# Kernel optimization log

Measured on AMD Instinct MI355X. Metric: run time of the kernel, lower is better.

## Reference

```python
import jax, jax.numpy as jnp
import numpy as np

NX = NY = NZ = 256   # linear_freqs
D1 = D2 = D3 = 8     # reduced_freqs
DF = 16              # feature_dim
NPTS = 131072


def softplus_b10(x):
    # torch F.softplus(x, beta=10, threshold=1)
    bx = 10.0 * x
    return jnp.where(bx > 1.0, x, 0.1 * jnp.log1p(jnp.exp(jnp.minimum(bx, 30.0))))


def grid_sample2d(vol, gx, gy):
    """Bilinear grid_sample, align_corners=True. vol:[C,H,W] (complex ok),
    gx,gy:[N] in [-1,1] (gx indexes W, gy indexes H). Returns [C,N]."""
    C, H, W = vol.shape
    ix = (gx + 1.0) * 0.5 * (W - 1)
    iy = (gy + 1.0) * 0.5 * (H - 1)
    x0f = jnp.floor(ix)
    y0f = jnp.floor(iy)
    wx = ix - x0f
    wy = iy - y0f
    x0 = jnp.clip(x0f.astype(jnp.int32), 0, W - 1)
    x1 = jnp.clip(x0 + 1, 0, W - 1)
    y0 = jnp.clip(y0f.astype(jnp.int32), 0, H - 1)
    y1 = jnp.clip(y0 + 1, 0, H - 1)
    v00 = vol[:, y0, x0]
    v01 = vol[:, y0, x1]
    v10 = vol[:, y1, x0]
    v11 = vol[:, y1, x1]
    return (v00 * (1 - wy) * (1 - wx) + v01 * (1 - wy) * wx
            + v10 * wy * (1 - wx) + v11 * wy * wx)


def batch_irfft(ph, x, ff, T):
    """ph:[D,d,N] complex, x:[N] in [-1,1], ff:[d] freqs. Returns [D,N]."""
    xx = (x + 1.0) * 0.5 * (T - 1) / T                    # [N]
    ang = 2.0 * np.pi * xx[:, None] * ff[None, :]         # [N,d]
    scale = jnp.where(ff > 0, 2.0, 1.0)
    tw_re = jnp.cos(ang) * scale
    tw_im = jnp.sin(ang) * scale
    return (jnp.einsum('dfn,nf->dn', ph.real, tw_re)
            - jnp.einsum('dfn,nf->dn', ph.imag, tw_im))


def setup_inputs() -> dict:
    key = jax.random.key(0)
    ks = jax.random.split(key, 8)
    inputs = jax.random.uniform(ks[0], (NPTS, 3), jnp.float32, minval=-1.0, maxval=1.0)
    s = 0.01
    Fx_re = jax.random.normal(ks[1], (1, DF, D1, NY, NZ), jnp.float32) * s
    Fx_im = jax.random.normal(ks[2], (1, DF, D1, NY, NZ), jnp.float32) * s
    Fy_re = jax.random.normal(ks[3], (1, DF, NX, D2, NZ), jnp.float32) * s
    Fy_im = jax.random.normal(ks[4], (1, DF, NX, D2, NZ), jnp.float32) * s
    Fz_re = jax.random.normal(ks[5], (1, DF, NX, NY, D3), jnp.float32) * s
    Fz_im = jax.random.normal(ks[6], (1, DF, NX, NY, D3), jnp.float32) * s
    alpha_params = jnp.array([0.001], jnp.float32)
    return {"inputs": inputs, "Fx_re": Fx_re, "Fx_im": Fx_im,
            "Fy_re": Fy_re, "Fy_im": Fy_im, "Fz_re": Fz_re, "Fz_im": Fz_im,
            "alpha_params": alpha_params}


def reference(inputs, Fx_re, Fx_im, Fy_re, Fy_im, Fz_re, Fz_im, alpha_params):
    alpha = softplus_b10(alpha_params)[0]
    Fx = (Fx_re + 1j * Fx_im) * alpha        # [1,D,d1,Ny,Nz]
    Fy = (Fy_re + 1j * Fy_im) * alpha        # [1,D,Nx,d2,Nz]
    Fz = (Fz_re + 1j * Fz_im) * alpha        # [1,D,Nx,Ny,d3]
    # inverse FFT over the two full (linear) spectral axes
    Fx = jnp.fft.ifftn(Fx, axes=(3, 4), norm='forward')
    Fy = jnp.fft.ifftn(Fy, axes=(2, 4), norm='forward')
    Fz = jnp.fft.ifftn(Fz, axes=(2, 3), norm='forward')
    xs, ys, zs = inputs[:, 0], inputs[:, 1], inputs[:, 2]
    N = inputs.shape[0]
    kx = jnp.arange(D1, dtype=jnp.float32)   # linear sampling axis [0,1,...]
    ky = jnp.arange(D2, dtype=jnp.float32)
    kz = jnp.arange(D3, dtype=jnp.float32)
    # complex bilinear gathers (H,W) = (Ny,Nz) / (Nx,Nz) / (Ny,Nx)
    fx = grid_sample2d(Fx.reshape(DF * D1, NY, NZ), zs, ys).reshape(DF, D1, N)
    fy = grid_sample2d(jnp.transpose(Fy, (0, 1, 3, 2, 4)).reshape(DF * D2, NX, NZ),
                       zs, xs).reshape(DF, D2, N)
    fz = grid_sample2d(jnp.transpose(Fz, (0, 1, 4, 3, 2)).reshape(DF * D3, NY, NX),
                       xs, ys).reshape(DF, D3, N)
    fxx = batch_irfft(fx, xs, kx, NX)
    fyy = batch_irfft(fy, ys, ky, NY)
    fzz = batch_irfft(fz, zs, kz, NZ)
    return (fxx + fyy + fzz).T               # [N, DF]
```

## Files before the change

kernel.cpp:

```cpp
#include <hip/hip_runtime.h>
#include <hip/hip_fp16.h>
#include <math.h>

#define NPTS 131072
#define RS 265
#define NBIN 65536

__device__ __forceinline__ float dev_alpha(const float* __restrict__ ap) {
    float x = ap[0];
    float bx = 10.0f * x;
    if (bx > 1.0f) return x;
    float e = expf(fminf(bx, 30.0f));
    return 0.1f * log1pf(e);
}

__device__ __forceinline__ void fft16_reg(float* re, float* im) {
    #define SW(a,b) { float t=re[a]; re[a]=re[b]; re[b]=t; t=im[a]; im[a]=im[b]; im[b]=t; }
    SW(1,8) SW(2,4) SW(3,12) SW(5,10) SW(7,14) SW(11,13)
    #undef SW
    const float C[8] = {1.f, 0.9238795325112867f, 0.7071067811865476f, 0.3826834323650898f,
                        0.f, -0.3826834323650898f, -0.7071067811865476f, -0.9238795325112867f};
    const float S[8] = {0.f, 0.3826834323650898f, 0.7071067811865476f, 0.9238795325112867f,
                        1.f, 0.9238795325112867f, 0.7071067811865476f, 0.3826834323650898f};
    #pragma unroll
    for (int m = 1; m < 16; m <<= 1) {
        #pragma unroll
        for (int k = 0; k < 16; k += 2 * m) {
            #pragma unroll
            for (int j = 0; j < m; ++j) {
                float wc = C[j * (8 / m)], ws = S[j * (8 / m)];
                int i0 = k + j, i1 = i0 + m;
                float tr = re[i1] * wc - im[i1] * ws;
                float ti = re[i1] * ws + im[i1] * wc;
                re[i1] = re[i0] - tr; im[i1] = im[i0] - ti;
                re[i0] += tr;         im[i0] += ti;
            }
        }
    }
}

__device__ __forceinline__ void fft256_block(float* lre, float* lim, int tid) {
    const int r = tid >> 4, s = tid & 15;
    float xr[16], xi[16];
    #pragma unroll
    for (int a = 0; a < 16; ++a) {
        xr[a] = lre[r * RS + 16 * a + s];
        xi[a] = lim[r * RS + 16 * a + s];
    }
    __syncthreads();
    fft16_reg(xr, xi);
    #pragma unroll
    for (int c = 0; c < 16; ++c) {
        float sn, cs;
        __sincosf(0.0245436926061703f * (float)(s * c), &sn, &cs);
        float tr = xr[c] * cs - xi[c] * sn;
        float ti = xr[c] * sn + xi[c] * cs;
        int idx = r * RS + 16 * c + (s ^ c);
        lre[idx] = tr; lim[idx] = ti;
    }
    __syncthreads();
    #pragma unroll
    for (int b = 0; b < 16; ++b) {
        int idx = r * RS + 16 * s + (b ^ s);
        xr[b] = lre[idx]; xi[b] = lim[idx];
    }
    __syncthreads();
    fft16_reg(xr, xi);
    #pragma unroll
    for (int d = 0; d < 16; ++d) {
        int idx = r * RS + 16 * d + s;
        lre[idx] = xr[d]; lim[idx] = xi[d];
    }
    __syncthreads();
}

__global__ __launch_bounds__(256) void fft_pass1_xy(
    const float* __restrict__ Fre, const float* __restrict__ Fim,
    const float* __restrict__ alpha_p, __half2* __restrict__ GT,
    int Sd, int Sa)
{
    __shared__ float lre[16 * RS], lim[16 * RS];
    const int tid = threadIdx.x, bg = blockIdx.x;
    const int d = bg & 7, ag = (bg >> 3) & 15, f = bg >> 7;
    const int a0 = ag * 16, c = f * 8 + d;
    const int base = f * 524288 + d * Sd + a0 * Sa;
    const float alpha = dev_alpha(alpha_p);
    for (int i = tid; i < 4096; i += 256) {
        int ar = i >> 8, b = i & 255;
        int addr = base + ar * Sa + b;
        lre[ar * RS + b] = Fre[addr] * alpha;
        lim[ar * RS + b] = Fim[addr] * alpha;
    }
    __syncthreads();
    fft256_block(lre, lim, tid);
    for (int i = tid; i < 4096; i += 256) {
        int k = i >> 4, rr = i & 15;
        GT[(c * 256 + k) * 256 + a0 + rr] = __floats2half2_rn(lre[rr * RS + k], lim[rr * RS + k]);
    }
}

__global__ __launch_bounds__(256) void fft_pass2_xy(
    const __half2* __restrict__ GT, __half2* __restrict__ V)
{
    __shared__ float lre[16 * RS], lim[16 * RS];
    const int tid = threadIdx.x, bg = blockIdx.x;
    const int cg = bg & 7, b = bg >> 3, c0 = cg * 16;
    for (int i = tid; i < 4096; i += 256) {
        int cr = i >> 8, a = i & 255;
        float2 v = __half22float2(GT[((c0 + cr) * 256 + b) * 256 + a]);
        lre[cr * RS + a] = v.x;
        lim[cr * RS + a] = v.y;
    }
    __syncthreads();
    fft256_block(lre, lim, tid);
    for (int i = tid; i < 4096; i += 256) {
        int k = i >> 4, cr = i & 15;
        V[(b * 256 + k) * 128 + c0 + cr] = __floats2half2_rn(lre[cr * RS + k], lim[cr * RS + k]);
    }
}

__global__ __launch_bounds__(256) void fft_pass1_z(
    const float* __restrict__ Fre, const float* __restrict__ Fim,
    const float* __restrict__ alpha_p, __half2* __restrict__ GTz)
{
    __shared__ float lre[16 * RS], lim[16 * RS];
    const int tid = threadIdx.x, bg = blockIdx.x;
    const int f = bg >> 7, kxp = bg & 127;
    const int base = f * 524288 + kxp * 4096;
    const float alpha = dev_alpha(alpha_p);
    for (int i = tid; i < 4096; i += 256) {
        int kxo = i >> 11, rem = i & 2047;
        int ky = rem >> 3, d = rem & 7;
        int row = kxo * 8 + d;
        lre[row * RS + ky] = Fre[base + i] * alpha;
        lim[row * RS + ky] = Fim[base + i] * alpha;
    }
    __syncthreads();
    fft256_block(lre, lim, tid);
    for (int i = tid; i < 4096; i += 256) {
        int k = i >> 4, rr = i & 15;
        GTz[k * 32768 + f * 2048 + kxp * 16 + rr] = __floats2half2_rn(lre[rr * RS + k], lim[rr * RS + k]);
    }
}

__global__ __launch_bounds__(256) void fft_pass2_z(
    const __half2* __restrict__ GTz, __half2* __restrict__ Vz)
{
    __shared__ float lre[16 * RS], lim[16 * RS];
    const int tid = threadIdx.x, bg = blockIdx.x;
    const int fp = bg & 7, b = bg >> 3;
    const int base = b * 32768 + fp * 4096;
    for (int i = tid; i < 4096; i += 256) {
        int fo = i >> 11, rem = i & 2047;
        int kx = rem >> 3, d = rem & 7;
        int row = fo * 8 + d;
        float2 v = __half22float2(GTz[base + i]);
        lre[row * RS + kx] = v.x;
        lim[row * RS + kx] = v.y;
    }
    __syncthreads();
    fft256_block(lre, lim, tid);
    for (int i = tid; i < 4096; i += 256) {
        int k = i >> 4, rr = i & 15;
        Vz[(b * 256 + k) * 128 + fp * 16 + rr] = __floats2half2_rn(lre[rr * RS + k], lim[rr * RS + k]);
    }
}

__device__ __forceinline__ int bin8(float v) {
    return min(max((int)((v + 1.0f) * 127.5f), 0), 255);
}
__device__ __forceinline__ int pt_key(const float* pts, int pid) {
    float y = pts[pid * 3 + 1], z = pts[pid * 3 + 2];
    return bin8(z) * 256 + bin8(y);
}

__global__ __launch_bounds__(256) void zero_hist(unsigned* __restrict__ h) {
    h[blockIdx.x * 256 + threadIdx.x] = 0;
}
__global__ __launch_bounds__(256) void hist_k(const float* __restrict__ pts, unsigned* __restrict__ h) {
    int pid = blockIdx.x * 256 + threadIdx.x;
    atomicAdd(&h[pt_key(pts, pid)], 1u);
}
__global__ __launch_bounds__(256) void scan_k(const unsigned* __restrict__ h, unsigned* __restrict__ cur) {
    __shared__ unsigned part[256];
    const int t = threadIdx.x;
    unsigned sum = 0;
    for (int i = 0; i < 256; ++i) sum += h[t * 256 + i];
    part[t] = sum;
    __syncthreads();
    for (int o = 1; o < 256; o <<= 1) {
        unsigned v = part[t];
        unsigned add = (t >= o) ? part[t - o] : 0u;
        __syncthreads();
        part[t] = v + add;
        __syncthreads();
    }
    unsigned run = (t > 0) ? part[t - 1] : 0u;
    for (int i = 0; i < 256; ++i) {
        cur[t * 256 + i] = run;
        run += h[t * 256 + i];
    }
}
__global__ __launch_bounds__(256) void scatter_k(const float* __restrict__ pts,
                                                 unsigned* __restrict__ cur,
                                                 unsigned* __restrict__ perm) {
    int pid = blockIdx.x * 256 + threadIdx.x;
    unsigned pos = atomicAdd(&cur[pt_key(pts, pid)], 1u);
    perm[pos] = (unsigned)pid;
}

__device__ __forceinline__ float4 bsample(const uint2* __restrict__ V,
                                          float gx, float gy, bool swap, int lane) {
    float ix = (gx + 1.0f) * 127.5f;
    float iy = (gy + 1.0f) * 127.5f;
    float x0f = floorf(ix), y0f = floorf(iy);
    float wx = ix - x0f, wy = iy - y0f;
    int x0 = min(max((int)x0f, 0), 255);
    int x1 = min(x0 + 1, 255);
    int y0 = min(max((int)y0f, 0), 255);
    int y1 = min(y0 + 1, 255);
    int rA, rB, rC, rD;
    if (swap) { rA = y0 * 256 + x0; rB = y0 * 256 + x1; rC = y1 * 256 + x0; rD = y1 * 256 + x1; }
    else      { rA = x0 * 256 + y0; rB = x1 * 256 + y0; rC = x0 * 256 + y1; rD = x1 * 256 + y1; }
    float w00 = (1.0f - wy) * (1.0f - wx);
    float w01 = (1.0f - wy) * wx;
    float w10 = wy * (1.0f - wx);
    float w11 = wy * wx;
    uint2 a = V[rA * 64 + lane];
    uint2 b = V[rB * 64 + lane];
    uint2 cc = V[rC * 64 + lane];
    uint2 dd = V[rD * 64 + lane];
    float4 s = make_float4(0.f, 0.f, 0.f, 0.f);
    float2 f0, f1;
    f0 = __half22float2(__builtin_bit_cast(__half2, a.x));  f1 = __half22float2(__builtin_bit_cast(__half2, a.y));
    s.x += w00 * f0.x; s.y += w00 * f0.y; s.z += w00 * f1.x; s.w += w00 * f1.y;
    f0 = __half22float2(__builtin_bit_cast(__half2, b.x));  f1 = __half22float2(__builtin_bit_cast(__half2, b.y));
    s.x += w01 * f0.x; s.y += w01 * f0.y; s.z += w01 * f1.x; s.w += w01 * f1.y;
    f0 = __half22float2(__builtin_bit_cast(__half2, cc.x)); f1 = __half22float2(__builtin_bit_cast(__half2, cc.y));
    s.x += w10 * f0.x; s.y += w10 * f0.y; s.z += w10 * f1.x; s.w += w10 * f1.y;
    f0 = __half22float2(__builtin_bit_cast(__half2, dd.x)); f1 = __half22float2(__builtin_bit_cast(__half2, dd.y));
    s.x += w11 * f0.x; s.y += w11 * f0.y; s.z += w11 * f1.x; s.w += w11 * f1.y;
    return s;
}

__device__ __forceinline__ float irdft(float4 s, float tw, int lane) {
    const float TWO_PI = 6.28318530717958647692f;
    float xx = (tw + 1.0f) * 0.5f * (255.0f / 256.0f);
    int k0 = (lane & 3) * 2;
    float sa, ca, sb, cb;
    __sincosf(TWO_PI * xx * (float)k0,       &sa, &ca);
    __sincosf(TWO_PI * xx * (float)(k0 + 1), &sb, &cb);
    float sc0 = (k0 > 0) ? 2.0f : 1.0f;
    return sc0 * (s.x * ca - s.y * sa) + 2.0f * (s.z * cb - s.w * sb);
}

__global__ __launch_bounds__(256) void sample_all(
    const uint2* __restrict__ Vx, const uint2* __restrict__ Vy, const uint2* __restrict__ Vz,
    const float* __restrict__ pts, const unsigned* __restrict__ perm,
    float* __restrict__ out)
{
    const int wid  = (int)((blockIdx.x * blockDim.x + threadIdx.x) >> 6);
    const int lane = threadIdx.x & 63;
    if (wid >= NPTS) return;
    const int pid = perm ? (int)perm[wid] : wid;
    const float xs = pts[pid * 3 + 0];
    const float ys = pts[pid * 3 + 1];
    const float zs = pts[pid * 3 + 2];

    float4 sx = bsample(Vx, zs, ys, false, lane);
    float4 sy = bsample(Vy, zs, xs, false, lane);
    float4 sz = bsample(Vz, xs, ys, true, lane);

    float p = irdft(sx, xs, lane) + irdft(sy, ys, lane) + irdft(sz, zs, lane);
    p += __shfl_xor(p, 1, 64);
    p += __shfl_xor(p, 2, 64);
    if ((lane & 3) == 0) out[pid * 16 + (lane >> 2)] = p;
}

extern "C" void kernel_launch(void* const* d_in, const int* in_sizes, int n_in,
                              void* d_out, int out_size, void* d_ws, size_t ws_size,
                              hipStream_t stream) {
    const float* pts     = (const float*)d_in[0];
    const float* Fx_re   = (const float*)d_in[1];
    const float* Fx_im   = (const float*)d_in[2];
    const float* Fy_re   = (const float*)d_in[3];
    const float* Fy_im   = (const float*)d_in[4];
    const float* Fz_re   = (const float*)d_in[5];
    const float* Fz_im   = (const float*)d_in[6];
    const float* alpha_p = (const float*)d_in[7];
    float* out = (float*)d_out;

    char* ws = (char*)d_ws;
    const size_t MB = 1024 * 1024;
    __half2* Vx = (__half2*)(ws);
    __half2* Vy = (__half2*)(ws + 32 * MB);
    __half2* Vz = (__half2*)(ws + 64 * MB);
    __half2* GT = (__half2*)(ws + 96 * MB);
    unsigned* hist = (unsigned*)(ws + 128 * MB);
    unsigned* cur  = (unsigned*)(ws + 128 * MB + 256 * 1024);
    unsigned* perm = (unsigned*)(ws + 128 * MB + 512 * 1024);
    const bool do_sort = ws_size >= 129 * MB + 64 * 1024;

    if (do_sort) {
        zero_hist<<<256, 256, 0, stream>>>(hist);
        hist_k<<<NPTS / 256, 256, 0, stream>>>(pts, hist);
        scan_k<<<1, 256, 0, stream>>>(hist, cur);
        scatter_k<<<NPTS / 256, 256, 0, stream>>>(pts, cur, perm);
    }

    fft_pass1_xy<<<2048, 256, 0, stream>>>(Fx_re, Fx_im, alpha_p, GT, 65536, 256);
    fft_pass2_xy<<<2048, 256, 0, stream>>>(GT, Vx);
    fft_pass1_xy<<<2048, 256, 0, stream>>>(Fy_re, Fy_im, alpha_p, GT, 256, 2048);
    fft_pass2_xy<<<2048, 256, 0, stream>>>(GT, Vy);
    fft_pass1_z<<<2048, 256, 0, stream>>>(Fz_re, Fz_im, alpha_p, GT);
    fft_pass2_z<<<2048, 256, 0, stream>>>(GT, Vz);

    sample_all<<<NPTS / 4, 256, 0, stream>>>((const uint2*)Vx, (const uint2*)Vy, (const uint2*)Vz,
                                             pts, do_sort ? perm : (const unsigned*)nullptr, out);
}
```

Measured before the change: 430.2 us.

## Vectorize FFT pass I/O, pack sorted points, use half2 bilinear math, swizzle blocks

The FFT passes now load float4 and half2x4 vectors and store 16-byte packed half2 outputs instead of scalar elements, and the shared-memory row stride changes from 265 to 264. The sort now scatters the point coordinates and original index into a packed float4 array, so the sampling kernel no longer does an indirect perm lookup followed by scattered coordinate loads. The sort also runs unconditionally, after the FFTs, reusing the GT scratch region. Bilinear interpolation accumulates in half2 FMA, and sample_all remaps block indices so concurrent blocks are spread across the sorted order. Risks include reduced precision from fp16 accumulation, bank conflicts from the even stride, and dropping the fallback for a small workspace.

```diff
diff --git a/kernel.cpp b/kernel.cpp
--- a/kernel.cpp
+++ b/kernel.cpp
@@ -3,8 +3,7 @@
 #include <math.h>
 
 #define NPTS 131072
-#define RS 265
-#define NBIN 65536
+#define RS 264
 
 __device__ __forceinline__ float dev_alpha(const float* __restrict__ ap) {
     float x = ap[0];
@@ -74,112 +73,159 @@
     __syncthreads();
 }
 
+__device__ __forceinline__ unsigned packh2(float re, float im) {
+    return __builtin_bit_cast(unsigned, __floats2half2_rn(re, im));
+}
+
 __global__ __launch_bounds__(256) void fft_pass1_xy(
-    const float* __restrict__ Fre, const float* __restrict__ Fim,
-    const float* __restrict__ alpha_p, __half2* __restrict__ GT,
-    int Sd, int Sa)
+    const float4* __restrict__ Fre4, const float4* __restrict__ Fim4,
+    const float* __restrict__ alpha_p, uint4* __restrict__ GT4,
+    int Sd4, int Sa4)
 {
     __shared__ float lre[16 * RS], lim[16 * RS];
     const int tid = threadIdx.x, bg = blockIdx.x;
     const int d = bg & 7, ag = (bg >> 3) & 15, f = bg >> 7;
     const int a0 = ag * 16, c = f * 8 + d;
-    const int base = f * 524288 + d * Sd + a0 * Sa;
+    const int base4 = f * 131072 + d * Sd4 + a0 * Sa4;
     const float alpha = dev_alpha(alpha_p);
-    for (int i = tid; i < 4096; i += 256) {
-        int ar = i >> 8, b = i & 255;
-        int addr = base + ar * Sa + b;
-        lre[ar * RS + b] = Fre[addr] * alpha;
-        lim[ar * RS + b] = Fim[addr] * alpha;
+    #pragma unroll
+    for (int j = 0; j < 4; ++j) {
+        int i4 = tid + 256 * j;
+        int ar = i4 >> 6, b4 = i4 & 63;
+        float4 vr = Fre4[base4 + ar * Sa4 + b4];
+        float4 vi = Fim4[base4 + ar * Sa4 + b4];
+        int o = ar * RS + 4 * b4;
+        lre[o+0]=vr.x*alpha; lre[o+1]=vr.y*alpha; lre[o+2]=vr.z*alpha; lre[o+3]=vr.w*alpha;
+        lim[o+0]=vi.x*alpha; lim[o+1]=vi.y*alpha; lim[o+2]=vi.z*alpha; lim[o+3]=vi.w*alpha;
     }
     __syncthreads();
     fft256_block(lre, lim, tid);
-    for (int i = tid; i < 4096; i += 256) {
-        int k = i >> 4, rr = i & 15;
-        GT[(c * 256 + k) * 256 + a0 + rr] = __floats2half2_rn(lre[rr * RS + k], lim[rr * RS + k]);
+    const int g = tid >> 2, rq = tid & 3;
+    #pragma unroll
+    for (int j = 0; j < 4; ++j) {
+        int k = g + 64 * j;
+        uint4 ov;
+        ov.x = packh2(lre[(4*rq+0)*RS+k], lim[(4*rq+0)*RS+k]);
+        ov.y = packh2(lre[(4*rq+1)*RS+k], lim[(4*rq+1)*RS+k]);
+        ov.z = packh2(lre[(4*rq+2)*RS+k], lim[(4*rq+2)*RS+k]);
+        ov.w = packh2(lre[(4*rq+3)*RS+k], lim[(4*rq+3)*RS+k]);
+        GT4[((c * 256 + k) * 256 + a0) / 4 + rq] = ov;
     }
 }
 
 __global__ __launch_bounds__(256) void fft_pass2_xy(
-    const __half2* __restrict__ GT, __half2* __restrict__ V)
+    const uint4* __restrict__ GT4, uint4* __restrict__ V4)
 {
     __shared__ float lre[16 * RS], lim[16 * RS];
     const int tid = threadIdx.x, bg = blockIdx.x;
     const int cg = bg & 7, b = bg >> 3, c0 = cg * 16;
-    for (int i = tid; i < 4096; i += 256) {
-        int cr = i >> 8, a = i & 255;
-        float2 v = __half22float2(GT[((c0 + cr) * 256 + b) * 256 + a]);
-        lre[cr * RS + a] = v.x;
-        lim[cr * RS + a] = v.y;
+    #pragma unroll
+    for (int j = 0; j < 4; ++j) {
+        int i4 = tid + 256 * j;
+        int cr = i4 >> 6, a4 = i4 & 63;
+        uint4 gv = GT4[(((c0 + cr) * 256 + b) * 256) / 4 + a4];
+        int o = cr * RS + 4 * a4;
+        float2 e;
+        e = __half22float2(__builtin_bit_cast(__half2, gv.x)); lre[o+0]=e.x; lim[o+0]=e.y;
+        e = __half22float2(__builtin_bit_cast(__half2, gv.y)); lre[o+1]=e.x; lim[o+1]=e.y;
+        e = __half22float2(__builtin_bit_cast(__half2, gv.z)); lre[o+2]=e.x; lim[o+2]=e.y;
+        e = __half22float2(__builtin_bit_cast(__half2, gv.w)); lre[o+3]=e.x; lim[o+3]=e.y;
     }
     __syncthreads();
     fft256_block(lre, lim, tid);
-    for (int i = tid; i < 4096; i += 256) {
-        int k = i >> 4, cr = i & 15;
-        V[(b * 256 + k) * 128 + c0 + cr] = __floats2half2_rn(lre[cr * RS + k], lim[cr * RS + k]);
+    const int g = tid >> 2, cq = tid & 3;
+    #pragma unroll
+    for (int j = 0; j < 4; ++j) {
+        int k = g + 64 * j;
+        uint4 ov;
+        ov.x = packh2(lre[(4*cq+0)*RS+k], lim[(4*cq+0)*RS+k]);
+        ov.y = packh2(lre[(4*cq+1)*RS+k], lim[(4*cq+1)*RS+k]);
+        ov.z = packh2(lre[(4*cq+2)*RS+k], lim[(4*cq+2)*RS+k]);
+        ov.w = packh2(lre[(4*cq+3)*RS+k], lim[(4*cq+3)*RS+k]);
+        V4[((b * 256 + k) * 128 + c0) / 4 + cq] = ov;
     }
 }
 
 __global__ __launch_bounds__(256) void fft_pass1_z(
-    const float* __restrict__ Fre, const float* __restrict__ Fim,
-    const float* __restrict__ alpha_p, __half2* __restrict__ GTz)
+    const float4* __restrict__ Fre4, const float4* __restrict__ Fim4,
+    const float* __restrict__ alpha_p, uint4* __restrict__ GTz4)
 {
     __shared__ float lre[16 * RS], lim[16 * RS];
     const int tid = threadIdx.x, bg = blockIdx.x;
     const int f = bg >> 7, kxp = bg & 127;
-    const int base = f * 524288 + kxp * 4096;
+    const int base4 = f * 131072 + kxp * 1024;
     const float alpha = dev_alpha(alpha_p);
-    for (int i = tid; i < 4096; i += 256) {
-        int kxo = i >> 11, rem = i & 2047;
-        int ky = rem >> 3, d = rem & 7;
-        int row = kxo * 8 + d;
-        lre[row * RS + ky] = Fre[base + i] * alpha;
-        lim[row * RS + ky] = Fim[base + i] * alpha;
+    #pragma unroll
+    for (int j = 0; j < 4; ++j) {
+        int i4 = tid + 256 * j;
+        int kxo = i4 >> 9, ky = (i4 & 511) >> 1, t0 = i4 & 1;
+        float4 vr = Fre4[base4 + i4];
+        float4 vi = Fim4[base4 + i4];
+        int row = kxo * 8 + 4 * t0;
+        lre[(row+0)*RS + ky] = vr.x*alpha; lim[(row+0)*RS + ky] = vi.x*alpha;
+        lre[(row+1)*RS + ky] = vr.y*alpha; lim[(row+1)*RS + ky] = vi.y*alpha;
+        lre[(row+2)*RS + ky] = vr.z*alpha; lim[(row+2)*RS + ky] = vi.z*alpha;
+        lre[(row+3)*RS + ky] = vr.w*alpha; lim[(row+3)*RS + ky] = vi.w*alpha;
     }
     __syncthreads();
     fft256_block(lre, lim, tid);
-    for (int i = tid; i < 4096; i += 256) {
-        int k = i >> 4, rr = i & 15;
-        GTz[k * 32768 + f * 2048 + kxp * 16 + rr] = __floats2half2_rn(lre[rr * RS + k], lim[rr * RS + k]);
+    const int g = tid >> 2, rq = tid & 3;
+    #pragma unroll
+    for (int j = 0; j < 4; ++j) {
+        int k = g + 64 * j;
+        uint4 ov;
+        ov.x = packh2(lre[(4*rq+0)*RS+k], lim[(4*rq+0)*RS+k]);
+        ov.y = packh2(lre[(4*rq+1)*RS+k], lim[(4*rq+1)*RS+k]);
+        ov.z = packh2(lre[(4*rq+2)*RS+k], lim[(4*rq+2)*RS+k]);
+        ov.w = packh2(lre[(4*rq+3)*RS+k], lim[(4*rq+3)*RS+k]);
+        GTz4[k * 8192 + f * 512 + kxp * 4 + rq] = ov;
     }
 }
 
 __global__ __launch_bounds__(256) void fft_pass2_z(
-    const __half2* __restrict__ GTz, __half2* __restrict__ Vz)
+    const uint4* __restrict__ GTz4, uint4* __restrict__ V4)
 {
     __shared__ float lre[16 * RS], lim[16 * RS];
     const int tid = threadIdx.x, bg = blockIdx.x;
     const int fp = bg & 7, b = bg >> 3;
-    const int base = b * 32768 + fp * 4096;
-    for (int i = tid; i < 4096; i += 256) {
-        int fo = i >> 11, rem = i & 2047;
-        int kx = rem >> 3, d = rem & 7;
-        int row = fo * 8 + d;
-        float2 v = __half22float2(GTz[base + i]);
-        lre[row * RS + kx] = v.x;
-        lim[row * RS + kx] = v.y;
+    const int base4 = b * 8192 + fp * 1024;
+    #pragma unroll
+    for (int j = 0; j < 4; ++j) {
+        int i4 = tid + 256 * j;
+        int fo = i4 >> 9, kx = (i4 & 511) >> 1, t0 = i4 & 1;
+        uint4 gv = GTz4[base4 + i4];
+        int row = fo * 8 + 4 * t0;
+        float2 e;
+        e = __half22float2(__builtin_bit_cast(__half2, gv.x)); lre[(row+0)*RS+kx]=e.x; lim[(row+0)*RS+kx]=e.y;
+        e = __half22float2(__builtin_bit_cast(__half2, gv.y)); lre[(row+1)*RS+kx]=e.x; lim[(row+1)*RS+kx]=e.y;
+        e = __half22float2(__builtin_bit_cast(__half2, gv.z)); lre[(row+2)*RS+kx]=e.x; lim[(row+2)*RS+kx]=e.y;
+        e = __half22float2(__builtin_bit_cast(__half2, gv.w)); lre[(row+3)*RS+kx]=e.x; lim[(row+3)*RS+kx]=e.y;
     }
     __syncthreads();
     fft256_block(lre, lim, tid);
-    for (int i = tid; i < 4096; i += 256) {
-        int k = i >> 4, rr = i & 15;
-        Vz[(b * 256 + k) * 128 + fp * 16 + rr] = __floats2half2_rn(lre[rr * RS + k], lim[rr * RS + k]);
+    const int g = tid >> 2, rq = tid & 3;
+    #pragma unroll
+    for (int j = 0; j < 4; ++j) {
+        int k = g + 64 * j;
+        uint4 ov;
+        ov.x = packh2(lre[(4*rq+0)*RS+k], lim[(4*rq+0)*RS+k]);
+        ov.y = packh2(lre[(4*rq+1)*RS+k], lim[(4*rq+1)*RS+k]);
+        ov.z = packh2(lre[(4*rq+2)*RS+k], lim[(4*rq+2)*RS+k]);
+        ov.w = packh2(lre[(4*rq+3)*RS+k], lim[(4*rq+3)*RS+k]);
+        V4[(b * 256 + k) * 32 + fp * 4 + rq] = ov;
     }
 }
 
 __device__ __forceinline__ int bin8(float v) {
     return min(max((int)((v + 1.0f) * 127.5f), 0), 255);
 }
-__device__ __forceinline__ int pt_key(const float* pts, int pid) {
-    float y = pts[pid * 3 + 1], z = pts[pid * 3 + 2];
-    return bin8(z) * 256 + bin8(y);
-}
-
 __global__ __launch_bounds__(256) void zero_hist(unsigned* __restrict__ h) {
     h[blockIdx.x * 256 + threadIdx.x] = 0;
 }
 __global__ __launch_bounds__(256) void hist_k(const float* __restrict__ pts, unsigned* __restrict__ h) {
     int pid = blockIdx.x * 256 + threadIdx.x;
-    atomicAdd(&h[pt_key(pts, pid)], 1u);
+    int key = bin8(pts[pid * 3 + 2]) * 256 + bin8(pts[pid * 3 + 1]);
+    atomicAdd(&h[key], 1u);
 }
 __global__ __launch_bounds__(256) void scan_k(const unsigned* __restrict__ h, unsigned* __restrict__ cur) {
     __shared__ unsigned part[256];
@@ -203,10 +249,12 @@
 }
 __global__ __launch_bounds__(256) void scatter_k(const float* __restrict__ pts,
                                                  unsigned* __restrict__ cur,
-                                                 unsigned* __restrict__ perm) {
+                                                 float4* __restrict__ ptsS) {
     int pid = blockIdx.x * 256 + threadIdx.x;
-    unsigned pos = atomicAdd(&cur[pt_key(pts, pid)], 1u);
-    perm[pos] = (unsigned)pid;
+    float x = pts[pid * 3 + 0], y = pts[pid * 3 + 1], z = pts[pid * 3 + 2];
+    int key = bin8(z) * 256 + bin8(y);
+    unsigned pos = atomicAdd(&cur[key], 1u);
+    ptsS[pos] = make_float4(x, y, z, __uint_as_float((unsigned)pid));
 }
 
 __device__ __forceinline__ float4 bsample(const uint2* __restrict__ V,
@@ -220,27 +268,26 @@
     int y0 = min(max((int)y0f, 0), 255);
     int y1 = min(y0 + 1, 255);
     int rA, rB, rC, rD;
-    if (swap) { rA = y0 * 256 + x0; rB = y0 * 256 + x1; rC = y1 * 256 + x0; rD = y1 * 256 + x1; }
-    else      { rA = x0 * 256 + y0; rB = x1 * 256 + y0; rC = x0 * 256 + y1; rD = x1 * 256 + y1; }
-    float w00 = (1.0f - wy) * (1.0f - wx);
-    float w01 = (1.0f - wy) * wx;
-    float w10 = wy * (1.0f - wx);
-    float w11 = wy * wx;
+    if (swap) { rA = y0*256+x0; rB = y0*256+x1; rC = y1*256+x0; rD = y1*256+x1; }
+    else      { rA = x0*256+y0; rB = x1*256+y0; rC = x0*256+y1; rD = x1*256+y1; }
     uint2 a = V[rA * 64 + lane];
     uint2 b = V[rB * 64 + lane];
-    uint2 cc = V[rC * 64 + lane];
-    uint2 dd = V[rD * 64 + lane];
-    float4 s = make_float4(0.f, 0.f, 0.f, 0.f);
-    float2 f0, f1;
-    f0 = __half22float2(__builtin_bit_cast(__half2, a.x));  f1 = __half22float2(__builtin_bit_cast(__half2, a.y));
-    s.x += w00 * f0.x; s.y += w00 * f0.y; s.z += w00 * f1.x; s.w += w00 * f1.y;
-    f0 = __half22float2(__builtin_bit_cast(__half2, b.x));  f1 = __half22float2(__builtin_bit_cast(__half2, b.y));
-    s.x += w01 * f0.x; s.y += w01 * f0.y; s.z += w01 * f1.x; s.w += w01 * f1.y;
-    f0 = __half22float2(__builtin_bit_cast(__half2, cc.x)); f1 = __half22float2(__builtin_bit_cast(__half2, cc.y));
-    s.x += w10 * f0.x; s.y += w10 * f0.y; s.z += w10 * f1.x; s.w += w10 * f1.y;
-    f0 = __half22float2(__builtin_bit_cast(__half2, dd.x)); f1 = __half22float2(__builtin_bit_cast(__half2, dd.y));
-    s.x += w11 * f0.x; s.y += w11 * f0.y; s.z += w11 * f1.x; s.w += w11 * f1.y;
-    return s;
+    uint2 c = V[rC * 64 + lane];
+    uint2 d = V[rD * 64 + lane];
+    __half2 w00 = __float2half2_rn((1.0f - wy) * (1.0f - wx));
+    __half2 w01 = __float2half2_rn((1.0f - wy) * wx);
+    __half2 w10 = __float2half2_rn(wy * (1.0f - wx));
+    __half2 w11 = __float2half2_rn(wy * wx);
+    __half2 acc0 = __hmul2(w00, __builtin_bit_cast(__half2, a.x));
+    __half2 acc1 = __hmul2(w00, __builtin_bit_cast(__half2, a.y));
+    acc0 = __hfma2(w01, __builtin_bit_cast(__half2, b.x), acc0);
+    acc1 = __hfma2(w01, __builtin_bit_cast(__half2, b.y), acc1);
+    acc0 = __hfma2(w10, __builtin_bit_cast(__half2, c.x), acc0);
+    acc1 = __hfma2(w10, __builtin_bit_cast(__half2, c.y), acc1);
+    acc0 = __hfma2(w11, __builtin_bit_cast(__half2, d.x), acc0);
+    acc1 = __hfma2(w11, __builtin_bit_cast(__half2, d.y), acc1);
+    return make_float4(__low2float(acc0), __high2float(acc0),
+                       __low2float(acc1), __high2float(acc1));
 }
 
 __device__ __forceinline__ float irdft(float4 s, float tw, int lane) {
@@ -256,25 +303,24 @@
 
 __global__ __launch_bounds__(256) void sample_all(
     const uint2* __restrict__ Vx, const uint2* __restrict__ Vy, const uint2* __restrict__ Vz,
-    const float* __restrict__ pts, const unsigned* __restrict__ perm,
-    float* __restrict__ out)
-{
-    const int wid  = (int)((blockIdx.x * blockDim.x + threadIdx.x) >> 6);
+    const float4* __restrict__ ptsS, float* __restrict__ out)
+{
+    const int lb = blockIdx.x;
+    const int chunk = (lb & 7) * 4096 + (lb >> 3);
+    const int wid = chunk * 4 + ((int)threadIdx.x >> 6);
     const int lane = threadIdx.x & 63;
-    if (wid >= NPTS) return;
-    const int pid = perm ? (int)perm[wid] : wid;
-    const float xs = pts[pid * 3 + 0];
-    const float ys = pts[pid * 3 + 1];
-    const float zs = pts[pid * 3 + 2];
+    float4 p = ptsS[wid];
+    const float xs = p.x, ys = p.y, zs = p.z;
+    const int pid = (int)__float_as_uint(p.w);
 
     float4 sx = bsample(Vx, zs, ys, false, lane);
     float4 sy = bsample(Vy, zs, xs, false, lane);
     float4 sz = bsample(Vz, xs, ys, true, lane);
 
-    float p = irdft(sx, xs, lane) + irdft(sy, ys, lane) + irdft(sz, zs, lane);
-    p += __shfl_xor(p, 1, 64);
-    p += __shfl_xor(p, 2, 64);
-    if ((lane & 3) == 0) out[pid * 16 + (lane >> 2)] = p;
+    float pv = irdft(sx, xs, lane) + irdft(sy, ys, lane) + irdft(sz, zs, lane);
+    pv += __shfl_xor(pv, 1, 64);
+    pv += __shfl_xor(pv, 2, 64);
+    if ((lane & 3) == 0) out[pid * 16 + (lane >> 2)] = pv;
 }
 
 extern "C" void kernel_launch(void* const* d_in, const int* in_sizes, int n_in,
@@ -292,29 +338,26 @@
 
     char* ws = (char*)d_ws;
     const size_t MB = 1024 * 1024;
-    __half2* Vx = (__half2*)(ws);
-    __half2* Vy = (__half2*)(ws + 32 * MB);
-    __half2* Vz = (__half2*)(ws + 64 * MB);
-    __half2* GT = (__half2*)(ws + 96 * MB);
-    unsigned* hist = (unsigned*)(ws + 128 * MB);
-    unsigned* cur  = (unsigned*)(ws + 128 * MB + 256 * 1024);
-    unsigned* perm = (unsigned*)(ws + 128 * MB + 512 * 1024);
-    const bool do_sort = ws_size >= 129 * MB + 64 * 1024;
-
-    if (do_sort) {
-        zero_hist<<<256, 256, 0, stream>>>(hist);
-        hist_k<<<NPTS / 256, 256, 0, stream>>>(pts, hist);
-        scan_k<<<1, 256, 0, stream>>>(hist, cur);
-        scatter_k<<<NPTS / 256, 256, 0, stream>>>(pts, cur, perm);
-    }
-
-    fft_pass1_xy<<<2048, 256, 0, stream>>>(Fx_re, Fx_im, alpha_p, GT, 65536, 256);
-    fft_pass2_xy<<<2048, 256, 0, stream>>>(GT, Vx);
-    fft_pass1_xy<<<2048, 256, 0, stream>>>(Fy_re, Fy_im, alpha_p, GT, 256, 2048);
-    fft_pass2_xy<<<2048, 256, 0, stream>>>(GT, Vy);
-    fft_pass1_z<<<2048, 256, 0, stream>>>(Fz_re, Fz_im, alpha_p, GT);
-    fft_pass2_z<<<2048, 256, 0, stream>>>(GT, Vz);
-
-    sample_all<<<NPTS / 4, 256, 0, stream>>>((const uint2*)Vx, (const uint2*)Vy, (const uint2*)Vz,
-                                             pts, do_sort ? perm : (const unsigned*)nullptr, out);
-}
+    uint4* Vx4 = (uint4*)(ws);
+    uint4* Vy4 = (uint4*)(ws + 32 * MB);
+    uint4* Vz4 = (uint4*)(ws + 64 * MB);
+    uint4* GT4 = (uint4*)(ws + 96 * MB);
+    unsigned* hist = (unsigned*)(ws + 96 * MB);
+    unsigned* cur  = (unsigned*)(ws + 96 * MB + 256 * 1024);
+    float4*   ptsS = (float4*)  (ws + 96 * MB + 512 * 1024);
+
+    fft_pass1_xy<<<2048, 256, 0, stream>>>((const float4*)Fx_re, (const float4*)Fx_im, alpha_p, GT4, 16384, 64);
+    fft_pass2_xy<<<2048, 256, 0, stream>>>(GT4, Vx4);
+    fft_pass1_xy<<<2048, 256, 0, stream>>>((const float4*)Fy_re, (const float4*)Fy_im, alpha_p, GT4, 64, 512);
+    fft_pass2_xy<<<2048, 256, 0, stream>>>(GT4, Vy4);
+    fft_pass1_z<<<2048, 256, 0, stream>>>((const float4*)Fz_re, (const float4*)Fz_im, alpha_p, GT4);
+    fft_pass2_z<<<2048, 256, 0, stream>>>(GT4, Vz4);
+
+    zero_hist<<<256, 256, 0, stream>>>(hist);
+    hist_k<<<NPTS / 256, 256, 0, stream>>>(pts, hist);
+    scan_k<<<1, 256, 0, stream>>>(hist, cur);
+    scatter_k<<<NPTS / 256, 256, 0, stream>>>(pts, cur, ptsS);
+
+    sample_all<<<NPTS / 4, 256, 0, stream>>>((const uint2*)Vx4, (const uint2*)Vy4, (const uint2*)Vz4,
+                                             ptsS, out);
+}
```

After: 384.0 us. 1.12x faster.
